# Optimization experiments

Measured on AMD Instinct MI355X. Metric: run time of the kernel, lower is better.

The kernel has to match this reference:

```python
import math
import jax
import jax.numpy as jnp
import numpy as np
from jax import lax

B_, L, D_MODEL = 2, 1024, 2048
D_STATE, D_CONV, EXPAND = 16, 4, 2
D_INNER = EXPAND * D_MODEL          # 4096
DT_RANK = math.ceil(D_MODEL / 16)   # 128


def setup_inputs() -> dict:
    key = jax.random.key(0)
    ks = jax.random.split(key, 8)
    hidden_states = jax.random.normal(ks[0], (B_, L, D_MODEL), jnp.float32)
    in_proj_w = jax.random.normal(ks[1], (2 * D_INNER, D_MODEL), jnp.float32) * (D_MODEL ** -0.5)
    conv_w = jax.random.normal(ks[2], (D_INNER, D_CONV), jnp.float32) * (D_CONV ** -0.5)
    conv_b = jnp.zeros((D_INNER,), jnp.float32)
    x_proj_w = jax.random.normal(ks[3], (DT_RANK + 2 * D_STATE, D_INNER), jnp.float32) * (D_INNER ** -0.5)
    dt_std = DT_RANK ** -0.5
    dt_proj_w = jax.random.uniform(ks[4], (D_INNER, DT_RANK), jnp.float32, minval=-dt_std, maxval=dt_std)
    # dt bias init: softplus^{-1} of dt sampled log-uniform in [1e-3, 1e-1]
    dt = jnp.exp(jax.random.uniform(ks[5], (D_INNER,), jnp.float32)
                 * (math.log(0.1) - math.log(0.001)) + math.log(0.001))
    dt = jnp.clip(dt, 1e-4)
    dt_proj_b = dt + jnp.log(-jnp.expm1(-dt))
    A_log = jnp.log(jnp.broadcast_to(jnp.arange(1, D_STATE + 1, dtype=jnp.float32), (D_INNER, D_STATE)))
    D = jnp.ones((D_INNER,), jnp.float32)
    out_proj_w = jax.random.normal(ks[6], (D_MODEL, D_INNER), jnp.float32) * (D_INNER ** -0.5)
    return {
        'hidden_states': hidden_states, 'in_proj_w': in_proj_w,
        'conv_w': conv_w, 'conv_b': conv_b, 'x_proj_w': x_proj_w,
        'dt_proj_w': dt_proj_w, 'dt_proj_b': dt_proj_b,
        'A_log': A_log, 'D': D, 'out_proj_w': out_proj_w,
    }


def _silu(v):
    return v * jax.nn.sigmoid(v)


def _mamba_forward(hidden_states, in_proj_w, conv_w, conv_b, x_proj_w,
                   dt_proj_w, dt_proj_b, A_log, D, out_proj_w):
    b, l, _ = hidden_states.shape
    # in_proj: (b,l,d_model) -> (b, 2*d_inner, l)
    xz = jnp.einsum('bld,ed->bel', hidden_states, in_proj_w)
    x, z = xz[:, :D_INNER, :], xz[:, D_INNER:, :]
    A = -jnp.exp(A_log.astype(jnp.float32))  # (d_inner, d_state)
    # causal depthwise conv1d + SiLU
    xp = jnp.pad(x, ((0, 0), (0, 0), (D_CONV - 1, 0)))
    x = lax.conv_general_dilated(
        xp, conv_w[:, None, :], window_strides=(1,), padding='VALID',
        dimension_numbers=('NCH', 'OIH', 'NCH'), feature_group_count=D_INNER)
    x = _silu(x + conv_b[None, :, None])  # (b, d_inner, l)
    # x_proj -> dt, B, C
    x_dbl = jnp.einsum('bdl,kd->blk', x, x_proj_w)  # (b,l,dt_rank+2n)
    dt_lo = x_dbl[..., :DT_RANK]
    Bmat = x_dbl[..., DT_RANK:DT_RANK + D_STATE]          # (b,l,n)
    Cmat = x_dbl[..., DT_RANK + D_STATE:]                 # (b,l,n)
    delta = jax.nn.softplus(jnp.einsum('blr,dr->bld', dt_lo, dt_proj_w)
                            + dt_proj_b.astype(jnp.float32))  # (b,l,d)
    xt = jnp.transpose(x, (2, 0, 1))       # (l,b,d)
    dl = jnp.transpose(delta, (1, 0, 2))   # (l,b,d)
    Bl = jnp.transpose(Bmat, (1, 0, 2))    # (l,b,n)
    Cl = jnp.transpose(Cmat, (1, 0, 2))    # (l,b,n)

    def step(h, inp):
        d_t, B_t, C_t, x_t = inp
        dA = jnp.exp(d_t[..., None] * A)                       # (b,d,n)
        h = h * dA + d_t[..., None] * B_t[:, None, :] * x_t[..., None]
        y_t = jnp.sum(h * C_t[:, None, :], axis=-1)            # (b,d)
        return h, y_t

    h0 = jnp.zeros((b, D_INNER, D_STATE), jnp.float32)
    _, ys = lax.scan(step, h0, (dl, Bl, Cl, xt))  # ys: (l,b,d)
    y = jnp.transpose(ys, (1, 0, 2))              # (b,l,d)
    y = y + jnp.transpose(x, (0, 2, 1)) * D[None, None, :]
    y = y * _silu(jnp.transpose(z, (0, 2, 1)))
    out = jnp.einsum('bld,ed->ble', y, out_proj_w)  # (b,l,d_model)
    return out


def reference(hidden_states, in_proj_w, conv_w, conv_b, x_proj_w,
              dt_proj_w, dt_proj_b, A_log, D, out_proj_w):
    return _mamba_forward(hidden_states, in_proj_w, conv_w, conv_b, x_proj_w,
                          dt_proj_w, dt_proj_b, A_log, D, out_proj_w)
```

## Files before the change

kernel.cpp:

```cpp
#include <hip/hip_runtime.h>
#include <hip/hip_bf16.h>
#include <stdint.h>

#define BB 2
#define LL 1024
#define DMODEL 2048
#define DINNER 4096
#define DSTATE 16
#define DTRANK 128
#define XDBL_LD 256
#define CHUNK 64
#define NCH (LL / CHUNK)

typedef unsigned short ushort;
using short8 = __attribute__((ext_vector_type(8))) short;
using f32x4  = __attribute__((ext_vector_type(4))) float;
using us4    = __attribute__((ext_vector_type(4))) ushort;

__device__ __forceinline__ float bf2f(ushort u) {
    union { uint32_t i; float f; } v; v.i = ((uint32_t)u) << 16; return v.f;
}
__device__ __forceinline__ ushort f2bf(float f) {
    union { float f; uint32_t i; } v; v.f = f;
    uint32_t lsb = (v.i >> 16) & 1u;
    uint32_t r = v.i + 0x7FFFu + lsb;
    return (ushort)(r >> 16);
}

__device__ __forceinline__ void glds16(const ushort* g, ushort* l) {
    __builtin_amdgcn_global_load_lds(
        (const __attribute__((address_space(1))) void*)g,
        (__attribute__((address_space(3))) void*)l,
        16, 0, 0);
}

__global__ __launch_bounds__(256) void cvt_all(
    const float4* __restrict__ hidden, const float4* __restrict__ inproj,
    const float4* __restrict__ dtw, const float4* __restrict__ outp,
    const float4* __restrict__ xproj,
    us4* __restrict__ hid_h, us4* __restrict__ inp_h, us4* __restrict__ dtp_h,
    us4* __restrict__ outp_h, us4* __restrict__ xpp)
{
    long i = (long)blockIdx.x * 256 + threadIdx.x;
    const float4* src; us4* dst; long j;
    if (i < 1048576)      { src = hidden; dst = hid_h;  j = i; }
    else if (i < 5242880) { src = inproj; dst = inp_h;  j = i - 1048576; }
    else if (i < 5373952) { src = dtw;    dst = dtp_h;  j = i - 5242880; }
    else if (i < 7471104) { src = outp;   dst = outp_h; j = i - 5373952; }
    else {
        j = i - 7471104; dst = xpp;
        if (j >= 163840) { us4 z = {0, 0, 0, 0}; dst[j] = z; return; }
        src = xproj;
    }
    float4 v = src[j];
    us4 o; o.x = f2bf(v.x); o.y = f2bf(v.y); o.z = f2bf(v.z); o.w = f2bf(v.w);
    dst[j] = o;
}

template <bool WF, bool WH>
__global__ __launch_bounds__(512, 2) void gemm_nt256(
    const ushort* __restrict__ A, int lda,
    const ushort* __restrict__ Bm, int ldb,
    float* __restrict__ Cf, ushort* __restrict__ Ch, int ldc,
    int K)
{
    __shared__ __align__(16) ushort sA[2][256 * 64];
    __shared__ __align__(16) ushort sB[2][256 * 64];

    const int tid  = threadIdx.x;
    const int lane = tid & 63;
    const int wave = tid >> 6;
    const int wr   = wave >> 2;
    const int wcol = wave & 3;
    const int lrow = lane & 15;
    const int lg   = lane >> 4;
    const int s7   = lane & 7;
    const int kb0 = ((0 + lg) ^ s7) << 4;
    const int kb1 = ((4 + lg) ^ s7) << 4;

    const int NT = gridDim.x, MT = gridDim.y;
    int mt, nt;
    if ((NT & 7) == 0) {
        int lin   = blockIdx.y * NT + blockIdx.x;
        int strip = NT >> 3;
        int xcd   = lin & 7;
        int idx   = lin >> 3;
        nt = xcd * strip + (idx % strip);
        mt = idx / strip;
    } else { mt = blockIdx.y; nt = blockIdx.x; }
    const long m0 = (long)mt * 256;
    const long n0 = (long)nt * 256;

    const long zoff = (long)blockIdx.z;
    A  += zoff * (long)K;
    Bm += zoff * (long)K;
    const long Mrows = (long)MT * 256;
    if (WF) Cf += zoff * Mrows * (long)ldc;

    f32x4 acc[8][4] = {};

    const int sr   = tid >> 3;
    const int scol = (((tid & 7) ^ (sr & 7)) << 3);
    const ushort* Ag = A  + (m0 + sr) * (long)lda + scol;
    const ushort* Bg = Bm + (n0 + sr) * (long)ldb + scol;

    const int NKT = K >> 6;

    {
        ushort* dA0 = &sA[0][0] + tid * 8;
        ushort* dB0 = &sB[0][0] + tid * 8;
        #pragma unroll
        for (int c = 0; c < 4; ++c) {
            glds16(Ag + (c * 64) * (long)lda, dA0 + c * 4096);
            glds16(Bg + (c * 64) * (long)ldb, dB0 + c * 4096);
        }
    }
    __syncthreads();

    const int arow0 = (wr * 128 + lrow) * 128;
    const int brow0 = (wcol * 64 + lrow) * 128;

    for (int kt = 0; kt < NKT; ++kt) {
        const int p = kt & 1;
        const char* sap = (const char*)&sA[p][0];
        const char* sbp = (const char*)&sB[p][0];
        ushort* dA = &sA[p ^ 1][0] + tid * 8;
        ushort* dB = &sB[p ^ 1][0] + tid * 8;
        const long kn = (long)(kt + 1) << 6;
        const bool pf = (kt + 1 < NKT);

        short8 bf[4][2];
        #pragma unroll
        for (int j = 0; j < 4; ++j) {
            const int bb = brow0 + (j * 16) * 128;
            bf[j][0] = *(const short8*)(sbp + bb + kb0);
            bf[j][1] = *(const short8*)(sbp + bb + kb1);
        }

        #pragma unroll
        for (int mh = 0; mh < 2; ++mh) {
            short8 af[4][2];
            #pragma unroll
            for (int i4 = 0; i4 < 4; ++i4) {
                const int ab = arow0 + (mh * 64 + i4 * 16) * 128;
                af[i4][0] = *(const short8*)(sap + ab + kb0);
                af[i4][1] = *(const short8*)(sap + ab + kb1);
            }
            if (pf) {
                if (mh == 0) {
                    #pragma unroll
                    for (int c = 0; c < 4; ++c)
                        glds16(Ag + (c * 64) * (long)lda + kn, dA + c * 4096);
                } else {
                    #pragma unroll
                    for (int c = 0; c < 4; ++c)
                        glds16(Bg + (c * 64) * (long)ldb + kn, dB + c * 4096);
                }
            }
            __builtin_amdgcn_s_setprio(1);
            #pragma unroll
            for (int ks = 0; ks < 2; ++ks)
                #pragma unroll
                for (int i4 = 0; i4 < 4; ++i4)
                    #pragma unroll
                    for (int j = 0; j < 4; ++j)
                        acc[mh * 4 + i4][j] =
                            __builtin_amdgcn_mfma_f32_16x16x32_bf16(
                                af[i4][ks], bf[j][ks],
                                acc[mh * 4 + i4][j], 0, 0, 0);
            __builtin_amdgcn_s_setprio(0);
        }
        __syncthreads();
    }

    const int r0 = (lane >> 4) * 4;
    const int c0 = lane & 15;
    #pragma unroll
    for (int i = 0; i < 8; ++i) {
        #pragma unroll
        for (int j = 0; j < 4; ++j) {
            const long col = n0 + wcol * 64 + j * 16 + c0;
            #pragma unroll
            for (int r = 0; r < 4; ++r) {
                const long row = m0 + wr * 128 + i * 16 + r0 + r;
                const float v = acc[i][j][r];
                const long idx = row * (long)ldc + col;
                if (WF) Cf[idx] = v;
                if (WH) Ch[idx] = f2bf(v);
            }
        }
    }
}

__global__ __launch_bounds__(512, 2) void gemm_delta(
    const ushort* __restrict__ A,
    const ushort* __restrict__ Bm,
    ushort* __restrict__ Ch,
    const float* __restrict__ bias)
{
    __shared__ __align__(16) ushort sA[128 * 128];
    __shared__ __align__(16) ushort sB[256 * 128];

    const int tid  = threadIdx.x;
    const int lane = tid & 63;
    const int wave = tid >> 6;
    const int wr   = wave >> 2;
    const int wcol = wave & 3;
    const int lrow = lane & 15;
    const int lg   = lane >> 4;
    const int s7r  = lrow & 7;

    const int NT = gridDim.x;
    int mt, nt;
    {
        int lin   = blockIdx.y * NT + blockIdx.x;
        int strip = NT >> 3;
        int xcd   = lin & 7;
        int idx   = lin >> 3;
        nt = xcd * strip + (idx % strip);
        mt = idx / strip;
    }
    const long m0 = (long)mt * 128;
    const long n0 = (long)nt * 256;

    const int srow = tid >> 4;
    const int scol = (((tid & 15) ^ ((tid >> 4) & 7)) << 3);
    const ushort* Ag = A  + (m0 + srow) * (long)XDBL_LD + scol;
    const ushort* Bg = Bm + (n0 + srow) * (long)DTRANK + scol;

    #pragma unroll
    for (int c = 0; c < 4; ++c)
        glds16(Ag + (c * 32) * (long)XDBL_LD, &sA[0] + c * 4096 + tid * 8);
    #pragma unroll
    for (int c = 0; c < 8; ++c)
        glds16(Bg + (c * 32) * (long)DTRANK, &sB[0] + c * 4096 + tid * 8);
    __syncthreads();

    f32x4 acc[4][4] = {};
    const char* sap = (const char*)&sA[0];
    const char* sbp = (const char*)&sB[0];
    const int arow0 = (wr * 64 + lrow) * 256;
    const int brow0 = (wcol * 64 + lrow) * 256;

    #pragma unroll
    for (int ks = 0; ks < 4; ++ks) {
        const int kb = ((ks * 4 + lg) ^ s7r) << 4;
        short8 af[4], bf[4];
        #pragma unroll
        for (int i = 0; i < 4; ++i)
            af[i] = *(const short8*)(sap + arow0 + (i * 16) * 256 + kb);
        #pragma unroll
        for (int j = 0; j < 4; ++j)
            bf[j] = *(const short8*)(sbp + brow0 + (j * 16) * 256 + kb);
        #pragma unroll
        for (int i = 0; i < 4; ++i)
            #pragma unroll
            for (int j = 0; j < 4; ++j)
                acc[i][j] = __builtin_amdgcn_mfma_f32_16x16x32_bf16(
                    af[i], bf[j], acc[i][j], 0, 0, 0);
    }

    const int r0 = (lane >> 4) * 4;
    const int c0 = lane & 15;
    #pragma unroll
    for (int i = 0; i < 4; ++i) {
        #pragma unroll
        for (int j = 0; j < 4; ++j) {
            const long col = n0 + wcol * 64 + j * 16 + c0;
            const float bv = bias[col];
            #pragma unroll
            for (int r = 0; r < 4; ++r) {
                const long row = m0 + wr * 64 + i * 16 + r0 + r;
                float v = acc[i][j][r] + bv;
                v = (v > 20.f) ? v : log1pf(__expf(v));
                Ch[row * (long)DINNER + col] = f2bf(v);
            }
        }
    }
}

template <int EPI, bool WF, bool WH>
__global__ __launch_bounds__(256) void gemm_nt(
    const ushort* __restrict__ A, int lda,
    const ushort* __restrict__ Bm, int ldb,
    float* __restrict__ Cf, ushort* __restrict__ Ch, int ldc,
    int K, const float* __restrict__ bias)
{
    __shared__ __align__(16) ushort sA[128 * 64];
    __shared__ __align__(16) ushort sB[128 * 64];

    const int tid  = threadIdx.x;
    const int lane = tid & 63;
    const int wave = tid >> 6;
    const int wr = wave >> 1, wc = wave & 1;

    const int NT = gridDim.x, MT = gridDim.y;
    int mt, nt;
    if ((NT & 7) == 0) {
        int lin   = blockIdx.y * NT + blockIdx.x;
        int strip = NT >> 3;
        int xcd   = lin & 7;
        int idx   = lin >> 3;
        nt = xcd * strip + (idx % strip);
        mt = idx / strip;
    } else { mt = blockIdx.y; nt = blockIdx.x; }
    const long m0 = (long)mt * 128;
    const long n0 = (long)nt * 128;

    const long zoff = (long)blockIdx.z;
    A  += zoff * (long)K;
    Bm += zoff * (long)K;
    const long Mrows = (long)MT * 128;
    if (WF) Cf += zoff * Mrows * (long)ldc;
    if (WH) Ch += zoff * Mrows * (long)ldc;

    f32x4 acc[4][4] = {};

    const int lrow = lane & 15;
    const int lko  = (lane >> 4) << 3;

    const int sr = tid >> 3;
    const int sc = (tid & 7) << 3;
    const ushort* Ag = A  + (m0 + sr) * (long)lda + sc;
    const ushort* Bg = Bm + (n0 + sr) * (long)ldb + sc;
    ushort* lA = sA + tid * 8;
    ushort* lB = sB + tid * 8;

    for (int k0 = 0; k0 < K; k0 += 64) {
        __syncthreads();
        #pragma unroll
        for (int c = 0; c < 4; ++c) {
            glds16(Ag + (c * 32) * (long)lda + k0, lA + c * 2048);
            glds16(Bg + (c * 32) * (long)ldb + k0, lB + c * 2048);
        }
        __syncthreads();

        #pragma unroll
        for (int ks = 0; ks < 2; ++ks) {
            short8 af[4], bf[4];
            #pragma unroll
            for (int i = 0; i < 4; ++i)
                af[i] = *(const short8*)&sA[(wr * 64 + i * 16 + lrow) * 64 + ks * 32 + lko];
            #pragma unroll
            for (int j = 0; j < 4; ++j)
                bf[j] = *(const short8*)&sB[(wc * 64 + j * 16 + lrow) * 64 + ks * 32 + lko];

            #pragma unroll
            for (int i = 0; i < 4; ++i)
                #pragma unroll
                for (int j = 0; j < 4; ++j)
                    acc[i][j] = __builtin_amdgcn_mfma_f32_16x16x32_bf16(
                        af[i], bf[j], acc[i][j], 0, 0, 0);
        }
    }

    const int r0 = (lane >> 4) * 4;
    const int c0 = lane & 15;
    #pragma unroll
    for (int i = 0; i < 4; ++i) {
        #pragma unroll
        for (int j = 0; j < 4; ++j) {
            long col = n0 + wc * 64 + j * 16 + c0;
            float bv = 0.f;
            if (EPI == 1) bv = bias[col];
            #pragma unroll
            for (int r = 0; r < 4; ++r) {
                long row = m0 + wr * 64 + i * 16 + r0 + r;
                float v = acc[i][j][r];
                if (EPI == 1) {
                    v += bv;
                    v = (v > 20.f) ? v : log1pf(__expf(v));
                }
                long idx = row * (long)ldc + col;
                if (WF) Cf[idx] = v;
                if (WH) Ch[idx] = f2bf(v);
            }
        }
    }
}

template <int NZ, bool WH_>
__global__ __launch_bounds__(256) void reduce_k(
    const float4* __restrict__ parts, long stride4, int n4,
    float4* __restrict__ outF, us4* __restrict__ outH)
{
    int i = blockIdx.x * 256 + threadIdx.x;
    if (i >= n4) return;
    float4 s = parts[i];
    #pragma unroll
    for (int z = 1; z < NZ; ++z) {
        float4 v = parts[(long)z * stride4 + i];
        s.x += v.x; s.y += v.y; s.z += v.z; s.w += v.w;
    }
    if (outF) outF[i] = s;
    if (WH_) {
        us4 o; o.x = f2bf(s.x); o.y = f2bf(s.y); o.z = f2bf(s.z); o.w = f2bf(s.w);
        outH[i] = o;
    }
}

__global__ __launch_bounds__(256) void conv_silu_kernel(
    const ushort* __restrict__ xz,
    const float* __restrict__ cw,
    const float* __restrict__ cb,
    ushort* __restrict__ xc)
{
    int gid = blockIdx.x * 256 + threadIdx.x;
    int d  = gid & (DINNER - 1);
    int rl = gid >> 12;
    int l  = rl & (LL - 1);
    float acc = cb[d];
    #pragma unroll
    for (int j = 0; j < 4; ++j) {
        int li = l - 3 + j;
        if (li >= 0)
            acc += cw[d * 4 + j] * bf2f(xz[(long)(rl - 3 + j) * 8192 + d]);
    }
    float s = acc / (1.f + __expf(-acc));
    xc[gid] = f2bf(s);
}

__global__ __launch_bounds__(256) void scan_p1(
    const ushort* __restrict__ delta,
    const ushort* __restrict__ xc,
    const float*  __restrict__ xdbl,
    const float*  __restrict__ A_log,
    float* __restrict__ Hbuf,
    float* __restrict__ sumdt_buf)
{
    __shared__ float sB[CHUNK * 16];
    const int tid = threadIdx.x;
    const int k = blockIdx.y, b = blockIdx.z;
    const int d = blockIdx.x * 256 + tid;
    const int row0 = b * LL + k * CHUNK;

    #pragma unroll
    for (int i = 0; i < 4; ++i) {
        int idx = i * 256 + tid;
        sB[idx] = xdbl[(long)(row0 + (idx >> 4)) * XDBL_LD + DTRANK + (idx & 15)];
    }
    __syncthreads();

    float A[DSTATE];
    const float4* Ap = (const float4*)(A_log + d * DSTATE);
    #pragma unroll
    for (int i = 0; i < 4; ++i) {
        float4 v = Ap[i];
        A[i*4+0] = -__expf(v.x); A[i*4+1] = -__expf(v.y);
        A[i*4+2] = -__expf(v.z); A[i*4+3] = -__expf(v.w);
    }

    float H[DSTATE];
    #pragma unroll
    for (int s = 0; s < DSTATE; ++s) H[s] = 0.f;
    float sumdt = 0.f;

    for (int t = 0; t < CHUNK; ++t) {
        const long row = row0 + t;
        const float dt = bf2f(delta[row * DINNER + d]);
        const float xv = bf2f(xc[row * DINNER + d]);
        const float dx = dt * xv;
        sumdt += dt;
        #pragma unroll
        for (int s = 0; s < DSTATE; ++s) {
            float dA = __expf(dt * A[s]);
            H[s] = H[s] * dA + dx * sB[t * 16 + s];
        }
    }

    const long o = ((long)(b * NCH + k) * DINNER + d) * DSTATE;
    float4* Ho = (float4*)(Hbuf + o);
    #pragma unroll
    for (int i = 0; i < 4; ++i) {
        float4 v; v.x = H[i*4+0]; v.y = H[i*4+1]; v.z = H[i*4+2]; v.w = H[i*4+3];
        Ho[i] = v;
    }
    sumdt_buf[(b * NCH + k) * DINNER + d] = sumdt;
}

__global__ __launch_bounds__(256) void scan_p2(
    const float* __restrict__ A_log,
    const float* __restrict__ sumdt_buf,
    float* __restrict__ Hbuf)
{
    int gid = blockIdx.x * 256 + threadIdx.x;
    int b = gid >> 16;
    int rem = gid & 65535;
    int d = rem >> 4, s = rem & 15;
    float A = -__expf(A_log[d * DSTATE + s]);
    float h = 0.f;
    for (int k = 0; k < NCH; ++k) {
        long idx = ((long)(b * NCH + k) * DINNER + d) * DSTATE + s;
        float Hk = Hbuf[idx];
        float sd = sumdt_buf[(b * NCH + k) * DINNER + d];
        Hbuf[idx] = h;
        h = h * __expf(A * sd) + Hk;
    }
}

__global__ __launch_bounds__(256) void scan_p3(
    const ushort* __restrict__ delta,
    const ushort* __restrict__ xc,
    const float*  __restrict__ xdbl,
    const ushort* __restrict__ xz,
    const float*  __restrict__ A_log,
    const float*  __restrict__ Dp,
    const float*  __restrict__ hin,
    ushort* __restrict__ y)
{
    __shared__ float sBC[CHUNK * 32];
    const int tid = threadIdx.x;
    const int k = blockIdx.y, b = blockIdx.z;
    const int d = blockIdx.x * 256 + tid;
    const int row0 = b * LL + k * CHUNK;

    #pragma unroll
    for (int i = 0; i < 8; ++i) {
        int idx = i * 256 + tid;
        sBC[idx] = xdbl[(long)(row0 + (idx >> 5)) * XDBL_LD + DTRANK + (idx & 31)];
    }
    __syncthreads();

    float A[DSTATE];
    const float4* Ap = (const float4*)(A_log + d * DSTATE);
    #pragma unroll
    for (int i = 0; i < 4; ++i) {
        float4 v = Ap[i];
        A[i*4+0] = -__expf(v.x); A[i*4+1] = -__expf(v.y);
        A[i*4+2] = -__expf(v.z); A[i*4+3] = -__expf(v.w);
    }
    const float Dd = Dp[d];

    float h[DSTATE];
    const float4* Hp = (const float4*)(hin + ((long)(b * NCH + k) * DINNER + d) * DSTATE);
    #pragma unroll
    for (int i = 0; i < 4; ++i) {
        float4 v = Hp[i];
        h[i*4+0] = v.x; h[i*4+1] = v.y; h[i*4+2] = v.z; h[i*4+3] = v.w;
    }

    for (int t = 0; t < CHUNK; ++t) {
        const long row = row0 + t;
        const float dt = bf2f(delta[row * DINNER + d]);
        const float xv = bf2f(xc[row * DINNER + d]);
        const float dx = dt * xv;
        float yt = 0.f;
        #pragma unroll
        for (int s = 0; s < DSTATE; ++s) {
            float dA = __expf(dt * A[s]);
            h[s] = h[s] * dA + dx * sBC[t * 32 + s];
            yt += h[s] * sBC[t * 32 + 16 + s];
        }
        yt += xv * Dd;
        const float zv = bf2f(xz[row * 8192 + DINNER + d]);
        yt *= zv / (1.f + __expf(-zv));
        y[row * DINNER + d] = f2bf(yt);
    }
}

extern "C" void kernel_launch(void* const* d_in, const int* in_sizes, int n_in,
                              void* d_out, int out_size, void* d_ws, size_t ws_size,
                              hipStream_t stream)
{
    const float* hidden    = (const float*)d_in[0];
    const float* in_proj   = (const float*)d_in[1];
    const float* conv_w    = (const float*)d_in[2];
    const float* conv_b    = (const float*)d_in[3];
    const float* x_proj    = (const float*)d_in[4];
    const float* dt_proj_w = (const float*)d_in[5];
    const float* dt_proj_b = (const float*)d_in[6];
    const float* A_log     = (const float*)d_in[7];
    const float* Dp        = (const float*)d_in[8];
    const float* out_proj  = (const float*)d_in[9];
    float* out = (float*)d_out;

    char* ws = (char*)d_ws;
    ushort* xz_h    = (ushort*)(ws);
    ushort* xc      = (ushort*)(ws + 33554432);
    ushort* xpp     = (ushort*)(ws + 50331648);
    float*  xdbl    = (float*)(ws + 52428800);
    ushort* xdblh   = (ushort*)(ws + 54525952);
    ushort* delta_h = (ushort*)(ws + 55574528);
    ushort* yb      = (ushort*)(ws + 72351744);
    ushort* hid_h   = (ushort*)(ws + 89128960);
    ushort* inp_h   = (ushort*)(ws + 97517568);
    float*  parts   = (float*)(ws + 97517568);
    float*  Hbuf    = (float*)(ws + 97517568);
    float*  sumdt   = (float*)(ws + 105906176);
    ushort* dtp_h   = (ushort*)(ws + 131072000);
    ushort* outp_h  = (ushort*)(ws + 132120576);
    float*  parts2  = (float*)(ws);

    const int M = BB * LL;

    cvt_all<<<30208, 256, 0, stream>>>(
        (const float4*)hidden, (const float4*)in_proj, (const float4*)dt_proj_w,
        (const float4*)out_proj, (const float4*)x_proj,
        (us4*)hid_h, (us4*)inp_h, (us4*)dtp_h, (us4*)outp_h, (us4*)xpp);

    gemm_nt256<false, true><<<dim3(8192 / 256, M / 256), 512, 0, stream>>>(
        hid_h, DMODEL, inp_h, DMODEL, nullptr, xz_h, 8192, DMODEL);

    conv_silu_kernel<<<(M * DINNER) / 256, 256, 0, stream>>>(xz_h, conv_w, conv_b, xc);

    gemm_nt<0, true, false><<<dim3(XDBL_LD / 128, M / 128, 16), 256, 0, stream>>>(
        xc, DINNER, xpp, DINNER, parts, nullptr, XDBL_LD, DINNER / 16, nullptr);
    reduce_k<16, true><<<(M * XDBL_LD / 4 + 255) / 256, 256, 0, stream>>>(
        (const float4*)parts, (long)M * XDBL_LD / 4, M * XDBL_LD / 4,
        (float4*)xdbl, (us4*)xdblh);

    gemm_delta<<<dim3(DINNER / 256, M / 128), 512, 0, stream>>>(
        xdblh, dtp_h, delta_h, dt_proj_b);

    scan_p1<<<dim3(DINNER / 256, NCH, BB), 256, 0, stream>>>(
        delta_h, xc, xdbl, A_log, Hbuf, sumdt);
    scan_p2<<<(BB * DINNER * DSTATE) / 256, 256, 0, stream>>>(
        A_log, sumdt, Hbuf);
    scan_p3<<<dim3(DINNER / 256, NCH, BB), 256, 0, stream>>>(
        delta_h, xc, xdbl, xz_h, A_log, Dp, Hbuf, yb);

    gemm_nt256<true, false><<<dim3(DMODEL / 256, M / 256, 4), 512, 0, stream>>>(
        yb, DINNER, outp_h, DINNER, parts2, nullptr, DMODEL, DINNER / 4);
    reduce_k<4, false><<<(M * DMODEL / 4 + 255) / 256, 256, 0, stream>>>(
        (const float4*)parts2, (long)M * DMODEL / 4, M * DMODEL / 4,
        (float4*)out, nullptr);
}
```

Before: 456.7 us.

## Split GEMM main loop into four quadrant phases with fine-grained vmcnt waits

Restructures the bf16 MFMA GEMM k-loop into four sub-phases, each covering one quadrant of the 8x4 accumulator tile. Global-to-LDS prefetch is issued in quarter pieces between them, with explicit s_waitcnt vmcnt and raw s_barrier calls replacing a single __syncthreads per iteration. The B tile rows are remapped so each half can be staged and read independently. This aims to overlap global loads with MFMA work and cut full-barrier stalls, but adds more barriers and relies on hand-tuned wait counts that could be wrong or serialize execution.

```diff
diff --git a/kernel.cpp b/kernel.cpp
--- a/kernel.cpp
+++ b/kernel.cpp
@@ -33,6 +33,11 @@
         (__attribute__((address_space(3))) void*)l,
         16, 0, 0);
 }
+
+#define BAR()  __builtin_amdgcn_s_barrier()
+#define WAITV(n) asm volatile("s_waitcnt vmcnt(" #n ")" ::: "memory")
+#define LGKM0() do { asm volatile("s_waitcnt lgkmcnt(0)" ::: "memory"); \
+                     __builtin_amdgcn_sched_barrier(0); } while (0)
 
 __global__ __launch_bounds__(256) void cvt_all(
     const float4* __restrict__ hidden, const float4* __restrict__ inproj,
@@ -101,76 +106,91 @@
 
     const int sr   = tid >> 3;
     const int scol = (((tid & 7) ^ (sr & 7)) << 3);
-    const ushort* Ag = A  + (m0 + sr) * (long)lda + scol;
-    const ushort* Bg = Bm + (n0 + sr) * (long)ldb + scol;
+    const ushort* Ag = A + (m0 + sr) * (long)lda + scol;
+    const int brow_s = ((sr >> 5) << 6) + (sr & 31);
+    const ushort* BgS = Bm + (n0 + brow_s) * (long)ldb + scol;
 
     const int NKT = K >> 6;
 
-    {
-        ushort* dA0 = &sA[0][0] + tid * 8;
-        ushort* dB0 = &sB[0][0] + tid * 8;
-        #pragma unroll
-        for (int c = 0; c < 4; ++c) {
-            glds16(Ag + (c * 64) * (long)lda, dA0 + c * 4096);
-            glds16(Bg + (c * 64) * (long)ldb, dB0 + c * 4096);
-        }
-    }
-    __syncthreads();
-
     const int arow0 = (wr * 128 + lrow) * 128;
-    const int brow0 = (wcol * 64 + lrow) * 128;
+    const int brow0 = (wcol >> 1) * 8192 + (((wcol & 1) << 5) + lrow) * 128;
+
+    auto stageA = [&](int h, ushort* dst, long koff) {
+        glds16(Ag + (h * 64) * (long)lda + koff,        dst + h * 4096 + tid * 8);
+        glds16(Ag + (h * 64 + 128) * (long)lda + koff,  dst + (h + 2) * 4096 + tid * 8);
+    };
+    auto stageB = [&](int h, ushort* dst, long koff) {
+        glds16(BgS + (32 * h) * (long)ldb + koff,       dst + (2 * h) * 4096 + tid * 8);
+        glds16(BgS + (128 + 32 * h) * (long)ldb + koff, dst + (2 * h + 1) * 4096 + tid * 8);
+    };
+
+    short8 af[4][2], bf0[2][2], bf1[2][2];
+
+    auto readA = [&](const char* sap, int mh) {
+        #pragma unroll
+        for (int i4 = 0; i4 < 4; ++i4) {
+            const int ab = arow0 + (mh * 64 + i4 * 16) * 128;
+            af[i4][0] = *(const short8*)(sap + ab + kb0);
+            af[i4][1] = *(const short8*)(sap + ab + kb1);
+        }
+    };
+    auto readB = [&](const char* sbp, int nh, short8 (*bfr)[2]) {
+        const int bb = brow0 + nh * 16384;
+        #pragma unroll
+        for (int j2 = 0; j2 < 2; ++j2) {
+            bfr[j2][0] = *(const short8*)(sbp + bb + j2 * (16 * 128) + kb0);
+            bfr[j2][1] = *(const short8*)(sbp + bb + j2 * (16 * 128) + kb1);
+        }
+    };
+    auto mfma16 = [&](int mh, int nh, short8 (*bfr)[2]) {
+        __builtin_amdgcn_s_setprio(1);
+        #pragma unroll
+        for (int ks = 0; ks < 2; ++ks)
+            #pragma unroll
+            for (int i4 = 0; i4 < 4; ++i4)
+                #pragma unroll
+                for (int j2 = 0; j2 < 2; ++j2)
+                    acc[mh * 4 + i4][nh * 2 + j2] =
+                        __builtin_amdgcn_mfma_f32_16x16x32_bf16(
+                            af[i4][ks], bfr[j2][ks],
+                            acc[mh * 4 + i4][nh * 2 + j2], 0, 0, 0);
+        __builtin_amdgcn_s_setprio(0);
+    };
+
+    stageA(0, &sA[0][0], 0);
+    stageB(0, &sB[0][0], 0);
+    stageB(1, &sB[0][0], 0);
+    stageA(1, &sA[0][0], 0);
+    WAITV(4);
+    BAR();
 
     for (int kt = 0; kt < NKT; ++kt) {
-        const int p = kt & 1;
-        const char* sap = (const char*)&sA[p][0];
-        const char* sbp = (const char*)&sB[p][0];
-        ushort* dA = &sA[p ^ 1][0] + tid * 8;
-        ushort* dB = &sB[p ^ 1][0] + tid * 8;
+        const char* sap = (const char*)&sA[kt & 1][0];
+        const char* sbp = (const char*)&sB[kt & 1][0];
+        ushort* dA = &sA[(kt & 1) ^ 1][0];
+        ushort* dB = &sB[(kt & 1) ^ 1][0];
         const long kn = (long)(kt + 1) << 6;
         const bool pf = (kt + 1 < NKT);
 
-        short8 bf[4][2];
-        #pragma unroll
-        for (int j = 0; j < 4; ++j) {
-            const int bb = brow0 + (j * 16) * 128;
-            bf[j][0] = *(const short8*)(sbp + bb + kb0);
-            bf[j][1] = *(const short8*)(sbp + bb + kb1);
-        }
-
-        #pragma unroll
-        for (int mh = 0; mh < 2; ++mh) {
-            short8 af[4][2];
-            #pragma unroll
-            for (int i4 = 0; i4 < 4; ++i4) {
-                const int ab = arow0 + (mh * 64 + i4 * 16) * 128;
-                af[i4][0] = *(const short8*)(sap + ab + kb0);
-                af[i4][1] = *(const short8*)(sap + ab + kb1);
-            }
-            if (pf) {
-                if (mh == 0) {
-                    #pragma unroll
-                    for (int c = 0; c < 4; ++c)
-                        glds16(Ag + (c * 64) * (long)lda + kn, dA + c * 4096);
-                } else {
-                    #pragma unroll
-                    for (int c = 0; c < 4; ++c)
-                        glds16(Bg + (c * 64) * (long)ldb + kn, dB + c * 4096);
-                }
-            }
-            __builtin_amdgcn_s_setprio(1);
-            #pragma unroll
-            for (int ks = 0; ks < 2; ++ks)
-                #pragma unroll
-                for (int i4 = 0; i4 < 4; ++i4)
-                    #pragma unroll
-                    for (int j = 0; j < 4; ++j)
-                        acc[mh * 4 + i4][j] =
-                            __builtin_amdgcn_mfma_f32_16x16x32_bf16(
-                                af[i4][ks], bf[j][ks],
-                                acc[mh * 4 + i4][j], 0, 0, 0);
-            __builtin_amdgcn_s_setprio(0);
-        }
-        __syncthreads();
+        readA(sap, 0);
+        readB(sbp, 0, bf0);
+        if (pf) { stageA(0, dA, kn); WAITV(4); } else { WAITV(2); }
+        BAR(); LGKM0();
+        mfma16(0, 0, bf0);
+
+        readB(sbp, 1, bf1);
+        if (pf) { stageB(0, dB, kn); WAITV(4); } else { WAITV(0); }
+        BAR(); LGKM0();
+        mfma16(0, 1, bf1);
+
+        readA(sap, 1);
+        if (pf) stageB(1, dB, kn);
+        BAR(); LGKM0();
+        mfma16(1, 0, bf0);
+
+        if (pf) { stageA(1, dA, kn); WAITV(4); }
+        BAR(); LGKM0();
+        mfma16(1, 1, bf1);
     }
 
     const int r0 = (lane >> 4) * 4;
```

After: 453.7 us. About the same (-0.7%).
